# Optimization experiments

Measured on AMD Instinct MI355X. Metric: run time of the kernel, lower is better.

The kernel has to match this reference:

```python
import jax, jax.numpy as jnp
import numpy as np

VOCAB = 1024
EMBED_DIM = 64
COMMIT_COST = 0.25


def setup_inputs() -> dict:
    key = jax.random.key(0)
    k1, k2 = jax.random.split(key)
    z_e = jax.random.normal(k1, (64, 64, 32, 32), dtype=jnp.float32)
    # nn.Embedding init: uniform(-1/vocab, 1/vocab)
    embedding = jax.random.uniform(
        k2, (VOCAB, EMBED_DIM), dtype=jnp.float32,
        minval=-1.0 / VOCAB, maxval=1.0 / VOCAB)
    return {"z_e": z_e, "embedding": embedding}


def reference(z_e, embedding):
    b, d, h, w = z_e.shape
    # [B,D,H,W] -> [N,D]
    flat_z = jnp.transpose(z_e, (0, 2, 3, 1)).reshape(-1, d)
    # squared L2 distances to each code: [N, V]
    distances = (
        jnp.sum(flat_z * flat_z, axis=1, keepdims=True)
        + jnp.sum(embedding * embedding, axis=1)
        - 2.0 * flat_z @ embedding.T
    )
    flat_indices = jnp.argmin(distances, axis=1)
    indices = flat_indices.reshape(b, h, w)
    # gather codes and restore [B,D,H,W]
    z_q = embedding[flat_indices].reshape(b, h, w, d)
    z_q = jnp.transpose(z_q, (0, 3, 1, 2))
    quantization_loss = jnp.mean((z_q - jax.lax.stop_gradient(z_e)) ** 2)
    commitment_loss = jnp.mean((z_e - jax.lax.stop_gradient(z_q)) ** 2) * COMMIT_COST
    z_q_st = z_e + jax.lax.stop_gradient(z_q - z_e)
    # perplexity over codebook usage
    counts = jnp.zeros((VOCAB,), dtype=jnp.float32).at[flat_indices].add(1.0)
    avg_probs = counts / flat_indices.shape[0]
    perplexity = jnp.exp(-jnp.sum(avg_probs * jnp.log(avg_probs + 1e-10)))
    return (z_q_st, indices, quantization_loss, commitment_loss, perplexity)
```

## Files before the change

### kernel.cpp

```cpp
#include <hip/hip_runtime.h>
#include <math.h>

#define VOCAB 1024
#define ED 64
#define NROWS 65536
#define NELEM 4194304
#define MARGIN 2.0e-4f

typedef __attribute__((ext_vector_type(8))) short short8;
typedef __attribute__((ext_vector_type(4))) float f32x4;

__device__ __forceinline__ unsigned f2bf(float f) {
    unsigned u = __float_as_uint(f);
    u += 0x7fff + ((u >> 16) & 1);
    return u >> 16;
}

__device__ __forceinline__ unsigned long long packkey(float d, int c) {
    unsigned f = __float_as_uint(d);
    unsigned sd = (f & 0x80000000u) ? ~f : (f | 0x80000000u);
    return ((unsigned long long)sd << 32) | (unsigned)c;
}


__global__ void vq_prep(const float* __restrict__ emb, float* __restrict__ e2f,
                        uint4* __restrict__ FB, unsigned* __restrict__ hist) {
    const int tid = blockIdx.x * 256 + threadIdx.x;
    if (tid < 1024) hist[tid] = 0u;

    if (tid < VOCAB) {
        const float4* src = (const float4*)(emb + tid * ED);
        double s = 0.0;
        #pragma unroll
        for (int g = 0; g < 16; ++g) {
            float4 f = src[g];
            s = fma((double)f.x, (double)f.x, s);
            s = fma((double)f.y, (double)f.y, s);
            s = fma((double)f.z, (double)f.z, s);
            s = fma((double)f.w, (double)f.w, s);
        }
        e2f[tid] = (float)s;
    }
    #pragma unroll
    for (int e = 0; e < 4; ++e) {
        const int i = e * 2048 + tid;
        const int n = i & 15, q = (i >> 4) & 3, kh = (i >> 6) & 1, T = i >> 7;
        const int code = T * 16 + n;
        const int k0 = kh * 32 + q * 8;
        const float4* sp = (const float4*)(emb + code * 64 + k0);
        float4 f0 = sp[0], f1 = sp[1];
        uint4 pk;
        pk.x = f2bf(f0.x) | (f2bf(f0.y) << 16);
        pk.y = f2bf(f0.z) | (f2bf(f0.w) << 16);
        pk.z = f2bf(f1.x) | (f2bf(f1.y) << 16);
        pk.w = f2bf(f1.z) | (f2bf(f1.w) << 16);
        FB[i] = pk;
    }
}

#define EDOT(i) { \
    const float4 a4 = za4[i]; \
    const float4 b4 = zb4[i]; \
    ma = fmaf(a4.x, e##i[0], ma); ma = fmaf(a4.y, e##i[1], ma); \
    ma = fmaf(a4.z, e##i[2], ma); ma = fmaf(a4.w, e##i[3], ma); \
    mb = fmaf(b4.x, e##i[0], mb); mb = fmaf(b4.y, e##i[1], mb); \
    mb = fmaf(b4.z, e##i[2], mb); mb = fmaf(b4.w, e##i[3], mb); }

__global__ __launch_bounds__(256, 2)
void vq_main(const float* __restrict__ z, const float* __restrict__ emb,
             const float* __restrict__ e2f, const uint4* __restrict__ FB,
             float* __restrict__ out, double* __restrict__ lossp,
             unsigned* __restrict__ hist) {
    __shared__ float e2s[1024];
    __shared__ float rowb1[64], rowb2[64];
    __shared__ int   rowi1[64];
    __shared__ float zs[64 * 64];
    __shared__ float znsh[64];
    __shared__ unsigned long long wkey[4][64];
    __shared__ int flrows[64];
    __shared__ int flcs;
    __shared__ double wls[4];

    const int t = threadIdx.x;
    const int w = t >> 6, lane = t & 63;
    const int q = lane >> 4, n_lo = lane & 15;
    const int bk = blockIdx.x;
    const int n0 = bk * 64;
    const int b  = n0 >> 10;
    const int sb = n0 & 1023;

    #pragma unroll
    for (int i = 0; i < 4; ++i) e2s[i * 256 + t] = e2f[i * 256 + t];

    short8 af[2];
    {
        const int s = sb + w * 16 + n_lo;
        const float* zp = z + (size_t)b * 65536 + s;
        #pragma unroll
        for (int kh = 0; kh < 2; ++kh) {
            short8 fr;
            #pragma unroll
            for (int j = 0; j < 8; ++j) {
                int d = kh * 32 + q * 8 + j;
                fr[j] = (short)f2bf(-2.0f * zp[d * 1024]);
            }
            af[kh] = fr;
        }
    }

    float b1[4], b2[4]; int i1[4];
    #pragma unroll
    for (int sl = 0; sl < 4; ++sl) { b1[sl] = 3.4e38f; b2[sl] = 3.4e38f; i1[sl] = 0; }

    __syncthreads();

    const short8* FBs = (const short8*)FB;
    #pragma unroll 4
    for (int T = 0; T < 64; ++T) {
        short8 bf0 = FBs[T * 128 + lane];
        short8 bf1 = FBs[T * 128 + 64 + lane];
        const int cb = T * 16 + n_lo;
        const float e2 = e2s[cb];
        f32x4 a; a[0] = e2; a[1] = e2; a[2] = e2; a[3] = e2;
        a = __builtin_amdgcn_mfma_f32_16x16x32_bf16(af[0], bf0, a, 0, 0, 0);
        a = __builtin_amdgcn_mfma_f32_16x16x32_bf16(af[1], bf1, a, 0, 0, 0);
        #pragma unroll
        for (int reg = 0; reg < 4; ++reg) {
            float s0 = a[reg];
            b2[reg] = __builtin_amdgcn_fmed3f(s0, b1[reg], b2[reg]);
            bool lt = s0 < b1[reg];
            i1[reg] = lt ? cb : i1[reg];
            b1[reg] = lt ? s0 : b1[reg];
        }
    }

    #pragma unroll
    for (int m = 1; m < 16; m <<= 1) {
        #pragma unroll
        for (int sl = 0; sl < 4; ++sl) {
            float ob1 = __shfl_xor(b1[sl], m, 64);
            int   oi1 = __shfl_xor(i1[sl], m, 64);
            float ob2 = __shfl_xor(b2[sl], m, 64);
            float lose = fmaxf(b1[sl], ob1);
            b2[sl] = fminf(fminf(b2[sl], ob2), lose);
            bool take = (ob1 < b1[sl]) || (ob1 == b1[sl] && oi1 < i1[sl]);
            b1[sl] = take ? ob1 : b1[sl];
            i1[sl] = take ? oi1 : i1[sl];
        }
    }
    if (n_lo == 0) {
        #pragma unroll
        for (int reg = 0; reg < 4; ++reg) {
            int row = w * 16 + q * 4 + reg;
            rowb1[row] = b1[reg];
            rowb2[row] = b2[reg];
            rowi1[row] = i1[reg];
        }
    }
    __syncthreads();

    if (t < 64) {
        const bool want = rowb2[t] < rowb1[t] + MARGIN;
        unsigned long long mask = __ballot(want);
        if (t == 0) flcs = __popcll(mask);
        if (want) {
            const int rank = __popcll(mask & ((1ULL << t) - 1ULL));
            flrows[rank] = t;
        }
    }
    __syncthreads();
    const int flc = flcs;

    if (flc > 0) {
        {
            const int fi = t >> 2, d0 = (t & 3) * 16;
            if (fi < flc) {
                const int r = flrows[fi];
                const float* zp = z + (size_t)b * 65536 + (size_t)d0 * 1024 + (sb + r);
                #pragma unroll
                for (int k = 0; k < 16; ++k)
                    zs[fi * 64 + d0 + k] = zp[(size_t)k * 1024];
            }
        }
        for (int i = t; i < 256; i += 256) wkey[i >> 6][i & 63] = ~0ULL;
        __syncthreads();
        if (t < flc) {
            const float* zp = zs + t * 64;
            double a = 0.0;
            for (int k = 0; k < 64; ++k) { const double v = (double)zp[k]; a = fma(v, v, a); }
            znsh[t] = (float)a;
        }
        __syncthreads();
        #pragma unroll 1
        for (int p = 0; p < 4; ++p) {
            const int c = p * 256 + w * 64 + lane;
            const f32x4* ep = (const f32x4*)(emb + (size_t)c * 64);
            f32x4 e0 = ep[0],  e1 = ep[1],  e2 = ep[2],  e3 = ep[3];
            f32x4 e4 = ep[4],  e5 = ep[5],  e6 = ep[6],  e7 = ep[7];
            f32x4 e8 = ep[8],  e9 = ep[9],  e10 = ep[10], e11 = ep[11];
            f32x4 e12 = ep[12], e13 = ep[13], e14 = ep[14], e15 = ep[15];
            const float e2c = e2s[c];
            #pragma unroll 1
            for (int r0 = 0; r0 < flc; r0 += 2) {
                const bool two = (r0 + 1 < flc);
                const float4* za4 = (const float4*)(zs + r0 * 64);
                const float4* zb4 = (const float4*)(zs + (two ? r0 + 1 : r0) * 64);
                float ma = 0.f, mb = 0.f;
                EDOT(0)  EDOT(1)  EDOT(2)  EDOT(3)
                EDOT(4)  EDOT(5)  EDOT(6)  EDOT(7)
                EDOT(8)  EDOT(9)  EDOT(10) EDOT(11)
                EDOT(12) EDOT(13) EDOT(14) EDOT(15)

                const float da = (znsh[r0] + e2c) - 2.0f * ma;
                unsigned long long ka = packkey(da, c);
                #pragma unroll
                for (int mo = 32; mo > 0; mo >>= 1) {
                    unsigned long long o = __shfl_xor(ka, mo, 64);
                    if (o < ka) ka = o;
                }
                if (lane == 0 && ka < wkey[w][r0]) wkey[w][r0] = ka;
                if (two) {
                    const float db = (znsh[r0 + 1] + e2c) - 2.0f * mb;
                    unsigned long long kb = packkey(db, c);
                    #pragma unroll
                    for (int mo = 32; mo > 0; mo >>= 1) {
                        unsigned long long o = __shfl_xor(kb, mo, 64);
                        if (o < kb) kb = o;
                    }
                    if (lane == 0 && kb < wkey[w][r0 + 1]) wkey[w][r0 + 1] = kb;
                }
            }
        }
        __syncthreads();
        if (t < flc) {
            unsigned long long k0 = wkey[0][t];
            #pragma unroll
            for (int i = 1; i < 4; ++i) {
                unsigned long long ki = wkey[i][t];
                if (ki < k0) k0 = ki;
            }
            rowi1[flrows[t]] = (int)(unsigned)(k0 & 0xffffffffu);
        }
        __syncthreads();
    }

    if (t < 64) {
        const int code = rowi1[t];
        out[NELEM + n0 + t] = (float)code;
        atomicAdd(&hist[code], 1u);
    }

    {
        const int r = lane;
        const int code2 = rowi1[r];
        const int scol = sb + r;
        double lsum = 0.0;
        #pragma unroll
        for (int i = 0; i < 4; ++i) {
            const int d4 = w * 4 + i;
            float4 e4 = *(const float4*)(emb + code2 * 64 + d4 * 4);
            float es[4] = {e4.x, e4.y, e4.z, e4.w};
            #pragma unroll
            for (int j = 0; j < 4; ++j) {
                int d = d4 * 4 + j;
                size_t off = (size_t)b * 65536 + (size_t)d * 1024 + scol;
                float zv = z[off];
                out[off] = zv + (es[j] - zv);
                double df = (double)es[j] - (double)zv;
                lsum = fma(df, df, lsum);
            }
        }
        #pragma unroll
        for (int off = 32; off > 0; off >>= 1)
            lsum += __shfl_down(lsum, off, 64);
        if (lane == 0) wls[w] = lsum;
    }
    __syncthreads();
    if (t == 0) lossp[bk] = wls[0] + wls[1] + wls[2] + wls[3];
}

__global__ void vq_finalize_kernel(const unsigned* __restrict__ hist,
                                   const double* __restrict__ lossp,
                                   float* __restrict__ out) {
    __shared__ double red[256], red2[256];
    int t = threadIdx.x;
    double ssum = 0.0, lsum = 0.0;
    for (int i = t; i < VOCAB; i += 256) {
        double p = (double)hist[i] / (double)NROWS;
        ssum += p * log(p + 1e-10);
    }
    for (int i = t; i < 1024; i += 256) lsum += lossp[i];
    red[t] = ssum; red2[t] = lsum;
    __syncthreads();
    for (int off = 128; off > 0; off >>= 1) {
        if (t < off) { red[t] += red[t + off]; red2[t] += red2[t + off]; }
        __syncthreads();
    }
    if (t == 0) {
        double qv = red2[0] / (double)NELEM;
        out[NELEM + NROWS + 0] = (float)qv;
        out[NELEM + NROWS + 1] = (float)(qv * 0.25);
        out[NELEM + NROWS + 2] = (float)exp(-red[0]);
    }
}

extern "C" void kernel_launch(void* const* d_in, const int* in_sizes, int n_in,
                              void* d_out, int out_size, void* d_ws, size_t ws_size,
                              hipStream_t stream) {
    const float* z   = (const float*)d_in[0];
    const float* emb = (const float*)d_in[1];
    float* out = (float*)d_out;

    float*    e2f   = (float*)d_ws;
    unsigned* hist  = (unsigned*)((char*)d_ws + 4096);
    uint4*    FB    = (uint4*)((char*)d_ws + 8192);
    double*   lossp = (double*)((char*)d_ws + 139264);

    vq_prep<<<dim3(8), dim3(256), 0, stream>>>(emb, e2f, FB, hist);
    vq_main<<<dim3(1024), dim3(256), 0, stream>>>(z, emb, e2f, FB, out, lossp, hist);
    vq_finalize_kernel<<<dim3(1), dim3(256), 0, stream>>>(hist, lossp, out);
}
```

Before: 164.2 us.

## Track top-3 candidates to narrow fp32 refinement to two-code checks for most rows

```diff
diff --git a/kernel.cpp b/kernel.cpp
--- a/kernel.cpp
+++ b/kernel.cpp
@@ -58,27 +58,18 @@
     }
 }
 
-#define EDOT(i) { \
-    const float4 a4 = za4[i]; \
-    const float4 b4 = zb4[i]; \
-    ma = fmaf(a4.x, e##i[0], ma); ma = fmaf(a4.y, e##i[1], ma); \
-    ma = fmaf(a4.z, e##i[2], ma); ma = fmaf(a4.w, e##i[3], ma); \
-    mb = fmaf(b4.x, e##i[0], mb); mb = fmaf(b4.y, e##i[1], mb); \
-    mb = fmaf(b4.z, e##i[2], mb); mb = fmaf(b4.w, e##i[3], mb); }
-
 __global__ __launch_bounds__(256, 2)
 void vq_main(const float* __restrict__ z, const float* __restrict__ emb,
              const float* __restrict__ e2f, const uint4* __restrict__ FB,
              float* __restrict__ out, double* __restrict__ lossp,
              unsigned* __restrict__ hist) {
     __shared__ float e2s[1024];
-    __shared__ float rowb1[64], rowb2[64];
-    __shared__ int   rowi1[64];
+    __shared__ float rowb1[64], rowb2[64], rowb3[64];
+    __shared__ int   rowi1[64], rowi2[64], rowfi[64];
     __shared__ float zs[64 * 64];
     __shared__ float znsh[64];
-    __shared__ unsigned long long wkey[4][64];
-    __shared__ int flrows[64];
-    __shared__ int flcs;
+    __shared__ int   flrows[64], frows2[64];
+    __shared__ int   flcs, nfulls;
     __shared__ double wls[4];
 
     const int t = threadIdx.x;
@@ -108,9 +99,12 @@
         }
     }
 
-    float b1[4], b2[4]; int i1[4];
+    float b1[4], b2[4], b3[4]; int i1[4], i2[4];
     #pragma unroll
-    for (int sl = 0; sl < 4; ++sl) { b1[sl] = 3.4e38f; b2[sl] = 3.4e38f; i1[sl] = 0; }
+    for (int sl = 0; sl < 4; ++sl) {
+        b1[sl] = 3.4e38f; b2[sl] = 3.4e38f; b3[sl] = 3.4e38f;
+        i1[sl] = 0; i2[sl] = 0;
+    }
 
     __syncthreads();
 
@@ -127,8 +121,11 @@
         #pragma unroll
         for (int reg = 0; reg < 4; ++reg) {
             float s0 = a[reg];
+            b3[reg] = __builtin_amdgcn_fmed3f(s0, b2[reg], b3[reg]);
+            bool lt2 = s0 < b2[reg];
+            bool lt  = s0 < b1[reg];
+            i2[reg] = lt2 ? (lt ? i1[reg] : cb) : i2[reg];
             b2[reg] = __builtin_amdgcn_fmed3f(s0, b1[reg], b2[reg]);
-            bool lt = s0 < b1[reg];
             i1[reg] = lt ? cb : i1[reg];
             b1[reg] = lt ? s0 : b1[reg];
         }
@@ -138,14 +135,23 @@
     for (int m = 1; m < 16; m <<= 1) {
         #pragma unroll
         for (int sl = 0; sl < 4; ++sl) {
-            float ob1 = __shfl_xor(b1[sl], m, 64);
-            int   oi1 = __shfl_xor(i1[sl], m, 64);
-            float ob2 = __shfl_xor(b2[sl], m, 64);
-            float lose = fmaxf(b1[sl], ob1);
-            b2[sl] = fminf(fminf(b2[sl], ob2), lose);
-            bool take = (ob1 < b1[sl]) || (ob1 == b1[sl] && oi1 < i1[sl]);
-            b1[sl] = take ? ob1 : b1[sl];
-            i1[sl] = take ? oi1 : i1[sl];
+            float oa1 = __shfl_xor(b1[sl], m, 64);
+            float oa2 = __shfl_xor(b2[sl], m, 64);
+            float oa3 = __shfl_xor(b3[sl], m, 64);
+            int   oj1 = __shfl_xor(i1[sl], m, 64);
+            int   oj2 = __shfl_xor(i2[sl], m, 64);
+            bool take = (oa1 < b1[sl]) || (oa1 == b1[sl] && oj1 < i1[sl]);
+            float w1  = take ? oa1 : b1[sl];  int ni1 = take ? oj1 : i1[sl];
+            float l1v = take ? b1[sl] : oa1;  int il1 = take ? i1[sl] : oj1;
+            float wt2 = take ? oa2 : b2[sl];  int iw2 = take ? oj2 : i2[sl];
+            float wt3 = take ? oa3 : b3[sl];
+            float lt2v = take ? b2[sl] : oa2;
+            bool t2 = wt2 < l1v;
+            float nb2 = t2 ? wt2 : l1v;       int ni2 = t2 ? iw2 : il1;
+            float nb3 = fminf(fmaxf(l1v, wt2), fminf(wt3, lt2v));
+            b1[sl] = w1;  i1[sl] = ni1;
+            b2[sl] = nb2; i2[sl] = ni2;
+            b3[sl] = nb3;
         }
     }
     if (n_lo == 0) {
@@ -154,35 +160,46 @@
             int row = w * 16 + q * 4 + reg;
             rowb1[row] = b1[reg];
             rowb2[row] = b2[reg];
+            rowb3[row] = b3[reg];
             rowi1[row] = i1[reg];
+            rowi2[row] = i2[reg];
         }
     }
     __syncthreads();
 
     if (t < 64) {
-        const bool want = rowb2[t] < rowb1[t] + MARGIN;
-        unsigned long long mask = __ballot(want);
-        if (t == 0) flcs = __popcll(mask);
-        if (want) {
-            const int rank = __popcll(mask & ((1ULL << t) - 1ULL));
-            flrows[rank] = t;
+        const float thr = rowb1[t] + MARGIN;
+        const bool pf = rowb2[t] < thr;
+        const bool ff = rowb3[t] < thr;
+        unsigned long long pm = __ballot(pf);
+        if (t == 0) flcs = __popcll(pm);
+        if (pf) {
+            const int rank = __popcll(pm & ((1ULL << t) - 1ULL));
+            flrows[rank] = t | (ff ? 256 : 0);
+            rowfi[t] = rank;
+        }
+        unsigned long long fm = __ballot(ff);
+        if (t == 0) nfulls = __popcll(fm);
+        if (ff) {
+            const int rank = __popcll(fm & ((1ULL << t) - 1ULL));
+            frows2[rank] = t;
         }
     }
     __syncthreads();
     const int flc = flcs;
+    const int nfull = nfulls;
 
     if (flc > 0) {
         {
             const int fi = t >> 2, d0 = (t & 3) * 16;
             if (fi < flc) {
-                const int r = flrows[fi];
+                const int r = flrows[fi] & 255;
                 const float* zp = z + (size_t)b * 65536 + (size_t)d0 * 1024 + (sb + r);
                 #pragma unroll
                 for (int k = 0; k < 16; ++k)
                     zs[fi * 64 + d0 + k] = zp[(size_t)k * 1024];
             }
         }
-        for (int i = t; i < 256; i += 256) wkey[i >> 6][i & 63] = ~0ULL;
         __syncthreads();
         if (t < flc) {
             const float* zp = zs + t * 64;
@@ -191,55 +208,64 @@
             znsh[t] = (float)a;
         }
         __syncthreads();
-        #pragma unroll 1
-        for (int p = 0; p < 4; ++p) {
-            const int c = p * 256 + w * 64 + lane;
-            const f32x4* ep = (const f32x4*)(emb + (size_t)c * 64);
-            f32x4 e0 = ep[0],  e1 = ep[1],  e2 = ep[2],  e3 = ep[3];
-            f32x4 e4 = ep[4],  e5 = ep[5],  e6 = ep[6],  e7 = ep[7];
-            f32x4 e8 = ep[8],  e9 = ep[9],  e10 = ep[10], e11 = ep[11];
-            f32x4 e12 = ep[12], e13 = ep[13], e14 = ep[14], e15 = ep[15];
-            const float e2c = e2s[c];
+
+        if (t < flc) {
+            const int ent = flrows[t];
+            if (!(ent & 256)) {
+                const int r = ent & 255;
+                const float zn = znsh[t];
+                const int c1 = rowi1[r], c2 = rowi2[r];
+                const float* zp = zs + t * 64;
+                const float4* e1p = (const float4*)(emb + (size_t)c1 * 64);
+                const float4* e2p = (const float4*)(emb + (size_t)c2 * 64);
+                float m1 = 0.f, m2 = 0.f;
+                #pragma unroll
+                for (int k4 = 0; k4 < 16; ++k4) {
+                    const float4 zz = *(const float4*)(zp + k4 * 4);
+                    const float4 ea = e1p[k4], eb = e2p[k4];
+                    m1 = fmaf(zz.x, ea.x, m1); m1 = fmaf(zz.y, ea.y, m1);
+                    m1 = fmaf(zz.z, ea.z, m1); m1 = fmaf(zz.w, ea.w, m1);
+                    m2 = fmaf(zz.x, eb.x, m2); m2 = fmaf(zz.y, eb.y, m2);
+                    m2 = fmaf(zz.z, eb.z, m2); m2 = fmaf(zz.w, eb.w, m2);
+                }
+                const float t1 = zn + e2s[c1];
+                const float t2v = zn + e2s[c2];
+                const float d1 = t1 - 2.0f * m1;
+                const float d2 = t2v - 2.0f * m2;
+                const int cw = (d2 < d1 || (d2 == d1 && c2 < c1)) ? c2 : c1;
+                rowi1[r] = cw;
+            }
+        }
+
+        for (int fj = w; fj < nfull; fj += 4) {
+            const int r = frows2[fj];
+            const int fi = rowfi[r];
+            const float zn = znsh[fi];
+            const float4* zz4 = (const float4*)(zs + fi * 64);
+            unsigned long long best = ~0ULL;
             #pragma unroll 1
-            for (int r0 = 0; r0 < flc; r0 += 2) {
-                const bool two = (r0 + 1 < flc);
-                const float4* za4 = (const float4*)(zs + r0 * 64);
-                const float4* zb4 = (const float4*)(zs + (two ? r0 + 1 : r0) * 64);
-                float ma = 0.f, mb = 0.f;
-                EDOT(0)  EDOT(1)  EDOT(2)  EDOT(3)
-                EDOT(4)  EDOT(5)  EDOT(6)  EDOT(7)
-                EDOT(8)  EDOT(9)  EDOT(10) EDOT(11)
-                EDOT(12) EDOT(13) EDOT(14) EDOT(15)
-
-                const float da = (znsh[r0] + e2c) - 2.0f * ma;
-                unsigned long long ka = packkey(da, c);
+            for (int j = 0; j < 16; ++j) {
+                const int c = j * 64 + lane;
+                const float4* ep4 = (const float4*)(emb + (size_t)c * 64);
+                float m = 0.f;
                 #pragma unroll
-                for (int mo = 32; mo > 0; mo >>= 1) {
-                    unsigned long long o = __shfl_xor(ka, mo, 64);
-                    if (o < ka) ka = o;
+                for (int k4 = 0; k4 < 16; ++k4) {
+                    const float4 e4v = ep4[k4];
+                    const float4 zz = zz4[k4];
+                    m = fmaf(zz.x, e4v.x, m); m = fmaf(zz.y, e4v.y, m);
+                    m = fmaf(zz.z, e4v.z, m); m = fmaf(zz.w, e4v.w, m);
                 }
-                if (lane == 0 && ka < wkey[w][r0]) wkey[w][r0] = ka;
-                if (two) {
-                    const float db = (znsh[r0 + 1] + e2c) - 2.0f * mb;
-                    unsigned long long kb = packkey(db, c);
-                    #pragma unroll
-                    for (int mo = 32; mo > 0; mo >>= 1) {
-                        unsigned long long o = __shfl_xor(kb, mo, 64);
-                        if (o < kb) kb = o;
-                    }
-                    if (lane == 0 && kb < wkey[w][r0 + 1]) wkey[w][r0 + 1] = kb;
-                }
-            }
-        }
-        __syncthreads();
-        if (t < flc) {
-            unsigned long long k0 = wkey[0][t];
+                const float tt = zn + e2s[c];
+                const float d = tt - 2.0f * m;
+                const unsigned long long kk = packkey(d, c);
+                if (kk < best) best = kk;
+            }
             #pragma unroll
-            for (int i = 1; i < 4; ++i) {
-                unsigned long long ki = wkey[i][t];
-                if (ki < k0) k0 = ki;
-            }
-            rowi1[flrows[t]] = (int)(unsigned)(k0 & 0xffffffffu);
+            for (int mo = 32; mo > 0; mo >>= 1) {
+                unsigned long long o = __shfl_xor(best, mo, 64);
+                if (o < best) best = o;
+            }
+            if (lane == 0) rowi1[r] = (int)(unsigned)(best & 0xffffffffu);
         }
         __syncthreads();
     }
```

After: 154.6 us, median of 3. 1.06x faster.
